# Performance work log

Measured on AMD Instinct MI355X. Metric: run time of the kernel, lower is better.

The kernel has to match this reference:

```python
import jax, jax.numpy as jnp
import numpy as np

I, H, M, C, LOC, K = 512, 256, 80, 1024, 32, 31
C2 = C // 2
B, S, T = 32, 256, 800


def setup_inputs() -> dict:
    key = jax.random.key(0)
    ks = jax.random.split(key, 20)
    sc = 0.02
    return {
        "encodings": jax.random.normal(ks[0], (B, S, I), jnp.float32),
        "queries": jax.random.normal(ks[1], (B, T, H), jnp.float32),
        "outputs": jax.random.normal(ks[2], (B, T, M), jnp.float32),
        "mask": jnp.ones((B, S), jnp.float32),
        # GRUCell (PyTorch layout: gates ordered r, z, n)
        "w_ih": jax.random.normal(ks[3], (3 * C, I + H), jnp.float32) * sc,
        "w_hh": jax.random.normal(ks[4], (3 * C, C), jnp.float32) * sc,
        "b_ih": jax.random.normal(ks[5], (3 * C,), jnp.float32) * sc,
        "b_hh": jax.random.normal(ks[6], (3 * C,), jnp.float32) * sc,
        "w_q": jax.random.normal(ks[7], (C2, C), jnp.float32) * sc,        # proj_query
        "w_loc1": jax.random.normal(ks[8], (LOC, 1, K), jnp.float32) * sc, # Conv1d(1, loc, K)
        "w_loc2": jax.random.normal(ks[9], (C2, LOC), jnp.float32) * sc,   # Conv1d(loc, C2, 1)
        "w_k": jax.random.normal(ks[10], (C2, I), jnp.float32) * sc,       # proj_key
        "b_k": jax.random.normal(ks[11], (C2,), jnp.float32) * sc,
        "w_agg": jax.random.normal(ks[12], (C2,), jnp.float32) * sc,       # Conv1d(C2, 1, 1)
        "w_t1": jax.random.normal(ks[13], (C, I + C + M), jnp.float32) * sc,
        "b_t1": jax.random.normal(ks[14], (C,), jnp.float32) * sc,
        "w_t2": jax.random.normal(ks[15], (C,), jnp.float32) * sc,
    }


def _conv1d(x, w, pad):
    # x: [B, Cin, S], w: [Cout, Cin, K]
    return jax.lax.conv_general_dilated(
        x, w, window_strides=(1,), padding=[(pad, pad)],
        dimension_numbers=("NCH", "OIH", "NCH"))


def _aligner(encodings, queries, outputs, maskb,
             w_ih, w_hh, b_ih, b_hh, w_q, w_loc1, w_loc2, w_k, b_k,
             w_agg, w_t1, b_t1, w_t2):
    bsize, seqlen, _ = encodings.shape
    # key projection: [B, S, C2]
    key = encodings @ w_k.T + b_k
    h0 = jnp.zeros((bsize, C), encodings.dtype)
    align0 = jnp.full((bsize, seqlen), 1.0 / seqlen, encodings.dtype)
    alpha0 = jnp.zeros((bsize, seqlen), encodings.dtype).at[:, 0].set(1.0)
    trans0 = jnp.full((bsize, 1), 0.5, encodings.dtype)

    def step(carry, xt):
        h, align, trans, alpha = carry
        query, frame = xt  # [B,H], [B,M]
        prev = jnp.einsum("bsi,bs->bi", encodings, alpha)
        x = jnp.concatenate([query, prev], axis=-1)  # [B, H+I]
        gx = x @ w_ih.T + b_ih
        gh = h @ w_hh.T + b_hh
        xr, xz, xn = jnp.split(gx, 3, axis=-1)
        hr, hz, hn = jnp.split(gh, 3, axis=-1)
        r = jax.nn.sigmoid(xr + hr)
        z = jax.nn.sigmoid(xz + hz)
        n = jnp.tanh(xn + r * hn)
        h_new = (1.0 - z) * n + z * h  # GRUCell update
        # location features: [B,1,S] -> [B,LOC,S] -> [B,C2,S]
        loc = _conv1d(align[:, None, :], w_loc1, K // 2)
        loc = jnp.einsum("cl,bls->bcs", w_loc2, loc)
        score = loc + (h_new @ w_q.T)[..., None] + key.swapaxes(1, 2)  # [B,C2,S]
        energy = jnp.einsum("c,bcs->bs", w_agg, jnp.tanh(score))
        energy = jnp.where(maskb, -jnp.inf, energy)
        align_new = jax.nn.softmax(energy, axis=-1)
        shifted = jnp.pad(alpha, ((0, 0), (1, 0)))[:, :-1]  # F.pad(alpha, [1,-1])
        alpha_new = ((1.0 - trans) * alpha + trans * shifted + 1e-7) * align_new
        alpha_new = alpha_new / alpha_new.sum(axis=-1, keepdims=True)
        attend = jnp.einsum("bsi,bs->bi", encodings, alpha_new)
        t_in = jnp.concatenate([attend, frame, h_new], axis=-1)
        t = jax.nn.sigmoid(jnp.tanh(t_in @ w_t1.T + b_t1) @ w_t2[:, None])  # [B,1]
        return (h_new, align_new, t, alpha_new), alpha_new

    xs = (queries.swapaxes(0, 1), outputs.swapaxes(0, 1))
    _, alphas = jax.lax.scan(step, (h0, align0, trans0, alpha0), xs)
    return alphas.swapaxes(0, 1)  # [B, T, S]


def reference(encodings, queries, outputs, mask,
              w_ih, w_hh, b_ih, b_hh, w_q, w_loc1, w_loc2, w_k, b_k,
              w_agg, w_t1, b_t1, w_t2):
    maskb = ~(mask.astype(bool))
    return _aligner(encodings, queries, outputs, maskb,
                    w_ih, w_hh, b_ih, b_hh, w_q, w_loc1, w_loc2, w_k, b_k,
                    w_agg, w_t1, b_t1, w_t2)
```

## Files before the change

### kernel.cpp

```cpp
#include <hip/hip_runtime.h>
#include <cstdint>
#include <cstddef>


namespace cfg {
constexpr int NB = 32, NS = 256, NI = 512, NHq = 256, NM = 80;
constexpr int NC = 1024, NC2 = 512, NT = 800;
constexpr int NBLK = 256, NTHR = 512;

constexpr size_t OFF_KEYT  = 0;
constexpr size_t OFF_WKT   = OFF_KEYT + (size_t)NB * NS * NC2;
constexpr size_t OFF_PU    = OFF_WKT + (size_t)NI * NC2;
constexpr size_t OFF_H     = OFF_PU + (size_t)2 * NB * NI;
constexpr size_t OFF_H16   = OFF_H + (size_t)2 * NC * NB;
constexpr size_t OFF_E     = OFF_H16 + (size_t)NB * NC;
constexpr size_t OFF_W     = OFF_E + (size_t)2 * NB * NS;
constexpr size_t OFF_SE    = OFF_W + (size_t)2 * NB * NS;
constexpr size_t OFF_SW    = OFF_SE + 64;
constexpr size_t OFF_TPART = OFF_SW + 64;
constexpr size_t OFF_TRED  = OFF_TPART + (size_t)NBLK * NB;
constexpr size_t OFF_QBUF  = OFF_TRED + 32;
constexpr size_t OFF_BAR   = OFF_QBUF + (size_t)NB * NC2;
constexpr size_t OFF_Q16   = OFF_BAR + 4608;
constexpr size_t OFF_F16   = OFF_Q16 + (size_t)NT * NB * NHq / 2;
constexpr size_t OFF_WQ16  = OFF_F16 + (size_t)NT * NB * 128 / 2;
constexpr size_t WS_FLOATS = OFF_WQ16 + (size_t)NC2 * NC / 2;
}
using namespace cfg;

typedef __attribute__((ext_vector_type(8))) short short8;
typedef __attribute__((ext_vector_type(4))) float f32x4;

#define MF(a, b, c) __builtin_amdgcn_mfma_f32_16x16x32_bf16((a), (b), (c), 0, 0, 0)
#define LDSC(d, p) asm volatile("global_load_dwordx4 %0, %1, off sc0 sc1" : "=v"(d) : "v"(p))

__device__ __forceinline__ float ld_cg(const float* p) {
  return __hip_atomic_load(p, __ATOMIC_RELAXED, __HIP_MEMORY_SCOPE_AGENT);
}
__device__ __forceinline__ void st_cg(float* p, float v) {
  __hip_atomic_store(p, v, __ATOMIC_RELAXED, __HIP_MEMORY_SCOPE_AGENT);
}
// ... 12 lines not shown
               : "+v"(a0), "+v"(a1), "+v"(a2), "+v"(a3), "+v"(a4), "+v"(a5), "+v"(a6), "+v"(a7));
}
__device__ __forceinline__ void vw10(short8& a0, short8& a1, short8& a2, short8& a3, short8& a4,
                                     short8& a5, short8& a6, short8& a7, short8& a8, short8& a9) {
  asm volatile("s_waitcnt vmcnt(0)"
               : "+v"(a0), "+v"(a1), "+v"(a2), "+v"(a3), "+v"(a4), "+v"(a5), "+v"(a6),
                 "+v"(a7), "+v"(a8), "+v"(a9));
}
__device__ __forceinline__ void vw15(short8& a0, short8& a1, short8& a2, short8& a3, short8& a4,
                                     short8& a5, short8& a6, short8& a7, short8& a8, short8& a9,
                                     short8& aa, short8& ab2, short8& ac, short8& ad, short8& ae) {
  asm volatile("s_waitcnt vmcnt(0)"
               : "+v"(a0), "+v"(a1), "+v"(a2), "+v"(a3), "+v"(a4), "+v"(a5), "+v"(a6),
                 "+v"(a7), "+v"(a8), "+v"(a9), "+v"(aa), "+v"(ab2), "+v"(ac), "+v"(ad), "+v"(ae));
}
__device__ __forceinline__ void vw16f(f32x4& a0, f32x4& a1, f32x4& a2, f32x4& a3, f32x4& a4,
                                      f32x4& a5, f32x4& a6, f32x4& a7, f32x4& b0, f32x4& b1,
                                      f32x4& b2, f32x4& b3, f32x4& b4, f32x4& b5, f32x4& b6,
                                      f32x4& b7) {
  asm volatile("s_waitcnt vmcnt(0)"
               : "+v"(a0), "+v"(a1), "+v"(a2), "+v"(a3), "+v"(a4), "+v"(a5), "+v"(a6), "+v"(a7),
                 "+v"(b0), "+v"(b1), "+v"(b2), "+v"(b3), "+v"(b4), "+v"(b5), "+v"(b6), "+v"(b7));
}

__device__ __forceinline__ float frcp(float x) {
#if __has_builtin(__builtin_amdgcn_rcpf)
  return __builtin_amdgcn_rcpf(x);
#else
  return 1.f / x;
#endif
}
__device__ __forceinline__ float fsig(float x) { return frcp(1.f + __expf(-x)); }
__device__ __forceinline__ float ftanh(float x) {
  const float e = __expf(2.f * x);
  return 1.f - 2.f * frcp(e + 1.f);
}
__device__ __forceinline__ short f2bf(float f) {
  unsigned u = __float_as_uint(f);
  u += 0x7FFFu + ((u >> 16) & 1u);
  return (short)(u >> 16);
}
__device__ __forceinline__ float bf2f(short s) {
  return __uint_as_float(((unsigned)(unsigned short)s) << 16);
}
__device__ __forceinline__ short8 cvt8(f32x4 lo, f32x4 hi) {
  short8 a;
  a[0] = f2bf(lo[0]); a[1] = f2bf(lo[1]); a[2] = f2bf(lo[2]); a[3] = f2bf(lo[3]);
  a[4] = f2bf(hi[0]); a[5] = f2bf(hi[1]); a[6] = f2bf(hi[2]); a[7] = f2bf(hi[3]);
  return a;
}

__device__ __forceinline__ void gbarrier(unsigned* root, unsigned* flags, unsigned& ph) {
  ++ph;
  asm volatile("s_waitcnt vmcnt(0)" ::: "memory");
  __syncthreads();
  if (blockIdx.x == 0) {
    const int t = threadIdx.x;
    if (t > 0 && t < 256) {
      while (__hip_atomic_load(&flags[t * 16], __ATOMIC_RELAXED, __HIP_MEMORY_SCOPE_AGENT) < ph)
        __builtin_amdgcn_s_sleep(1);
    }
    __syncthreads();
    if (t == 0)
      __hip_atomic_store(root, ph, __ATOMIC_RELAXED, __HIP_MEMORY_SCOPE_AGENT);
// ... 20 lines not shown
  if (k >= 256 && k < 768) return w_t1[(size_t)c * 1616 + (k - 256)];
  if (k >= 768 && k < 1792) return w_t1[(size_t)c * 1616 + 592 + (k - 768)];
  if (k >= 1792 && k < 1872) return w_t1[(size_t)c * 1616 + 512 + (k - 1792)];
  return 0.f;
}

__global__ void k_init(const float* __restrict__ enc, const float* __restrict__ queries,
                       const float* __restrict__ outputs, const float* __restrict__ w_k,
                       const float* __restrict__ w_q, float* __restrict__ ws) {
  const size_t t0 = (size_t)blockIdx.x * blockDim.x + threadIdx.x;
  const size_t gs = (size_t)gridDim.x * blockDim.x;
  for (size_t x = t0; x < (size_t)NI * NC2; x += gs) {
    const int i = (int)(x / NC2), c2 = (int)(x % NC2);
    ws[OFF_WKT + x] = w_k[(size_t)c2 * NI + i];
  }
  for (size_t x = t0; x < (size_t)NB * NI; x += gs) {
    const int b = (int)(x / NI), i = (int)(x % NI);
    ws[OFF_PU + x] = 0.f;
    ws[OFF_PU + (size_t)NB * NI + b * NI + i] = enc[(size_t)b * NS * NI + i];
  }
  for (size_t x = t0; x < (size_t)2 * NC * NB; x += gs) ws[OFF_H + x] = 0.f;
  for (size_t x = t0; x < (size_t)NB * NC; x += gs) ws[OFF_H16 + x] = 0.f;
  for (size_t x = t0; x < (size_t)NB * NS; x += gs) {
    ws[OFF_E + x] = 0.f;
    ws[OFF_E + (size_t)NB * NS + x] = 1.f;
    ws[OFF_W + x] = 0.f;
    ws[OFF_W + (size_t)NB * NS + x] = ((x & (NS - 1)) == 0) ? 1.f : 0.f;
  }
  for (size_t x = t0; x < (size_t)NB; x += gs) {
    ws[OFF_SE + x] = 0.f; ws[OFF_SE + NB + x] = (float)NS;
    ws[OFF_SW + x] = 0.f; ws[OFF_SW + NB + x] = 1.f;
    ws[OFF_TRED + x] = 0.f;
  }
  unsigned* bar = (unsigned*)(ws + OFF_BAR);
  for (size_t x = t0; x < 4608; x += gs) bar[x] = 0u;
  unsigned short* Q16 = (unsigned short*)(ws + OFF_Q16);
  for (size_t x = t0; x < (size_t)NT * NB * NHq; x += gs) {
    const int k = (int)(x & (NHq - 1));
    const int b = (int)((x >> 8) & (NB - 1));
    const int t = (int)(x >> 13);
    Q16[x] = (unsigned short)f2bf(queries[((size_t)b * NT + t) * NHq + k]);
  }
  unsigned short* F16 = (unsigned short*)(ws + OFF_F16);
  for (size_t x = t0; x < (size_t)NT * NB * 128; x += gs) {
    const int k = (int)(x & 127);
    const int b = (int)((x >> 7) & (NB - 1));
    const int t = (int)(x >> 12);
    F16[x] = (k < NM) ? (unsigned short)f2bf(outputs[((size_t)b * NT + t) * NM + k]) : 0;
  }
  unsigned short* WQ16 = (unsigned short*)(ws + OFF_WQ16);
  for (size_t x = t0; x < (size_t)NC2 * NC; x += gs)
    WQ16[x] = (unsigned short)f2bf(w_q[x]);
}

__global__ __launch_bounds__(NTHR) void k_key(const float* __restrict__ enc,
                                              const float* __restrict__ b_k,
                                              float* __restrict__ ws) {
  __shared__ float encl[4 * NI];
  const int bid = blockIdx.x, tid = threadIdx.x;
  const int b = bid >> 3, s0 = (bid & 7) * 32;
  const float* wkT = ws + OFF_WKT;
  float* keyT = ws + OFF_KEYT;
  const float bk = b_k[tid];
  for (int q = 0; q < 8; ++q) {
    const int sb = s0 + q * 4;
    for (int x = tid; x < 4 * NI; x += NTHR) {
      const int ss = x >> 9, i = x & (NI - 1);
      encl[x] = enc[((size_t)(b * NS + sb + ss)) * NI + i];
    }
    __syncthreads();
    float a0 = bk, a1 = bk, a2 = bk, a3 = bk;
    for (int i = 0; i < NI; ++i) {
      const float wv = wkT[(size_t)i * NC2 + tid];
      a0 += wv * encl[i];           a1 += wv * encl[NI + i];
      a2 += wv * encl[2 * NI + i];  a3 += wv * encl[3 * NI + i];
    }
    keyT[((size_t)(b * NS + sb + 0)) * NC2 + tid] = a0;
    keyT[((size_t)(b * NS + sb + 1)) * NC2 + tid] = a1;
    keyT[((size_t)(b * NS + sb + 2)) * NC2 + tid] = a2;
    keyT[((size_t)(b * NS + sb + 3)) * NC2 + tid] = a3;
    __syncthreads();
  }
}

__global__ __launch_bounds__(NTHR, 2) void k_main(
    const float* __restrict__ enc, const float* __restrict__ mask,
    const float* __restrict__ w_ih, const float* __restrict__ w_hh,
    const float* __restrict__ b_ih, const float* __restrict__ b_hh,
    const float* __restrict__ w_loc1, const float* __restrict__ w_loc2,
    const float* __restrict__ w_agg, const float* __restrict__ w_t1,
    const float* __restrict__ b_t1, const float* __restrict__ w_t2,
    float* ws, float* __restrict__ out) {
  const int bid = blockIdx.x, tid = threadIdx.x;
  float* const keyT = ws + OFF_KEYT;
  float* const PU = ws + OFF_PU;
  float* const HB = ws + OFF_H;
  unsigned short* const HB16 = (unsigned short*)(ws + OFF_H16);
  float* const EB = ws + OFF_E;
  float* const WBUF = ws + OFF_W;
  float* const SEB = ws + OFF_SE;
  float* const SWB = ws + OFF_SW;
  float* const TPART = ws + OFF_TPART;
  float* const TRED = ws + OFF_TRED;
  float* const QBUF = ws + OFF_QBUF;
  unsigned* const root = (unsigned*)(ws + OFF_BAR);
  unsigned* const flags = root + 16;
  const unsigned short* const Q16 = (const unsigned short*)(ws + OFF_Q16);
  const unsigned short* const F16 = (const unsigned short*)(ws + OFF_F16);
  const unsigned short* const WQ16 = (const unsigned short*)(ws + OFF_WQ16);

  __shared__ float Cred[2 * 5 * 4 * 64];
  __shared__ float gout2[5 * 4 * 32];
  __shared__ float swinv_l[32];
  __shared__ float tredl[128];
  __shared__ float alignl[72];
  __shared__ float wl2[34];
  __shared__ float qbl[520];
  __shared__ float Epart[32 * 9];
  __shared__ float wstash[32];
  __shared__ float scal[4];

  const int lane = tid & 63, wv = tid >> 6;
  const int m2 = wv >> 2, k4 = wv & 3;
  const int kg = lane >> 4;
  const int ab = m2 * 16 + (lane & 15);
  const int cs = bid * 4;
  const int pb_b = bid >> 3, pb_s0 = (bid & 7) * 32;
  const int col = lane & 15, quad = lane >> 4;
  unsigned ph = 0;

  short8 wreg[16];
  {
    const int n = lane & 15;
    const int kind = n >> 2, ch = cs + (n & 3);
#pragma unroll
    for (int si = 0; si < 16; ++si) {
      int s = (k4 == 0) ? (si < 8 ? si : (si < 15 ? 16 + si : -1))
            : (k4 == 1) ? 8 + si
            : (k4 == 2) ? (si < 15 ? 31 + si : -1)
                        : (si < 14 ? 46 + si : -1);
      short8 w = {0, 0, 0, 0, 0, 0, 0, 0};
      if (s >= 0) {
        const int k0 = s * 32 + kg * 8;
#pragma unroll
        for (int jj = 0; jj < 8; ++jj)
          w[jj] = f2bf(wcat_val(w_ih, w_hh, w_t1, kind, ch, k0 + jj));
      }
      wreg[si] = w;
    }
  }
  short8 wcA[4];
  unsigned keylo[4][2], keyhi[4][2];
  f32x4 wagr[4];
#pragma unroll
  for (int t = 0; t < 4; ++t) {
    const int mt = 4 * wv + t;
    short8 wfr;
#pragma unroll
    for (int jj = 0; jj < 8; ++jj) {
      const int k = quad * 8 + jj;
      float s = 0.f;
      if (k < 31) {
        const int c2 = mt * 16 + col;
        for (int l = 0; l < 32; ++l) s += w_loc2[c2 * 32 + l] * w_loc1[l * 31 + k];
      }
      wfr[jj] = f2bf(s);
    }
    wcA[t] = wfr;
    const int c2r = mt * 16 + quad * 4;
#pragma unroll
    for (int r = 0; r < 4; ++r) wagr[t][r] = w_agg[c2r + r];
#pragma unroll
    for (int nt = 0; nt < 2; ++nt) {
      const float* kp = &keyT[((size_t)(pb_b * NS + pb_s0 + nt * 16 + col)) * NC2 + c2r];
      keylo[t][nt] = ((unsigned)(unsigned short)f2bf(kp[0])) |
                     (((unsigned)(unsigned short)f2bf(kp[1])) << 16);
      keyhi[t][nt] = ((unsigned)(unsigned short)f2bf(kp[2])) |
                     (((unsigned)(unsigned short)f2bf(kp[3])) << 16);
    }
  }
  if (tid >= 62 && tid < 72) alignl[tid] = 0.f;
  __syncthreads();

  for (int j = 0; j < NT; ++j) {
    const int p = j & 1;
    const float* pu_prev = PU + (size_t)(1 - p) * NB * NI;
    float* pu_cur = PU + (size_t)p * NB * NI;
    const float* h_prev = HB + (size_t)(1 - p) * NC * NB;
    float* h_cur = HB + (size_t)p * NC * NB;
    const unsigned short* hb16_prev = HB16 + (size_t)(1 - p) * NB * NC;
    unsigned short* hb16_cur = HB16 + (size_t)p * NB * NC;
    const float* e_prev = EB + (size_t)(1 - p) * NB * NS;
    float* e_cur = EB + (size_t)p * NB * NS;
    const float* w_prev = WBUF + (size_t)(1 - p) * NB * NS;
    float* w_cur = WBUF + (size_t)p * NB * NS;
    const float* se_prev = SEB + (size_t)(1 - p) * NB;
    float* se_cur = SEB + (size_t)p * NB;
    const float* sw_prev = SWB + (size_t)(1 - p) * NB;
    float* sw_cur = SWB + (size_t)p * NB;

    if (tid < 64) st_cg(&pu_cur[bid * 64 + tid], 0.f);
    if (bid == 0 && tid < NB) st_cg(&se_cur[tid], 0.f);
    if (bid == 1 && tid < NB) st_cg(&sw_cur[tid], 0.f);
    if (tid < NB) swinv_l[tid] = 1.f / ld_cg(&sw_prev[tid]);
    __syncthreads();

    if (j >= 1 && bid < NB && tid < NS)
      out[((size_t)bid * NT + (j - 1)) * NS + tid] = ld_cg(&w_prev[bid * NS + tid]) * swinv_l[bid];

    f32x4 accA = {0.f, 0.f, 0.f, 0.f}, accB = {0.f, 0.f, 0.f, 0.f};
    if (k4 == 0) {
      const unsigned short* qp = Q16 + ((size_t)j * NB + ab) * NHq + kg * 8;
      const unsigned short* hp = hb16_prev + (size_t)ab * NC + kg * 8;
      short8 h0, h1, h2, h3, h4, h5, h6;
      LDSC(h0, hp);        LDSC(h1, hp + 32);   LDSC(h2, hp + 64);  LDSC(h3, hp + 96);
      LDSC(h4, hp + 128);  LDSC(h5, hp + 160);  LDSC(h6, hp + 192);
      const short8 q0 = *(const short8*)(qp);
      const short8 q1 = *(const short8*)(qp + 32);
      const short8 q2 = *(const short8*)(qp + 64);
      const short8 q3 = *(const short8*)(qp + 96);
      const short8 q4 = *(const short8*)(qp + 128);
      const short8 q5 = *(const short8*)(qp + 160);
      const short8 q6 = *(const short8*)(qp + 192);
      const short8 q7 = *(const short8*)(qp + 224);
      vw7(h0, h1, h2, h3, h4, h5, h6);
      accA = MF(q0, wreg[0], accA); accA = MF(q1, wreg[1], accA);
      accA = MF(q2, wreg[2], accA); accA = MF(q3, wreg[3], accA);
      accA = MF(q4, wreg[4], accA); accA = MF(q5, wreg[5], accA);
      accA = MF(q6, wreg[6], accA); accA = MF(q7, wreg[7], accA);
      accB = MF(h0, wreg[8], accB);  accB = MF(h1, wreg[9], accB);
      accB = MF(h2, wreg[10], accB); accB = MF(h3, wreg[11], accB);
      accB = MF(h4, wreg[12], accB); accB = MF(h5, wreg[13], accB);
      accB = MF(h6, wreg[14], accB);
    } else if (k4 == 1) {
      const float* pp = pu_prev + (size_t)ab * NI + kg * 8;
#pragma unroll
      for (int rd = 0; rd < 2; ++rd) {
        const float* pb = pp + rd * 256;
        f32x4 a0, a1, a2, a3, a4, a5, a6, a7, b0, b1, b2, b3, b4, b5, b6, b7;
        LDSC(a0, pb);        LDSC(b0, pb + 4);
        LDSC(a1, pb + 32);   LDSC(b1, pb + 36);
        LDSC(a2, pb + 64);   LDSC(b2, pb + 68);
        LDSC(a3, pb + 96);   LDSC(b3, pb + 100);
        LDSC(a4, pb + 128);  LDSC(b4, pb + 132);
        LDSC(a5, pb + 160);  LDSC(b5, pb + 164);
        LDSC(a6, pb + 192);  LDSC(b6, pb + 196);
        LDSC(a7, pb + 224);  LDSC(b7, pb + 228);
        vw16f(a0, a1, a2, a3, a4, a5, a6, a7, b0, b1, b2, b3, b4, b5, b6, b7);
        const int w0 = rd * 8;
        accA = MF(cvt8(a0, b0), wreg[w0 + 0], accA);
        accA = MF(cvt8(a1, b1), wreg[w0 + 1], accA);
        accA = MF(cvt8(a2, b2), wreg[w0 + 2], accA);
        accA = MF(cvt8(a3, b3), wreg[w0 + 3], accA);
        accA = MF(cvt8(a4, b4), wreg[w0 + 4], accA);
        accA = MF(cvt8(a5, b5), wreg[w0 + 5], accA);
        accA = MF(cvt8(a6, b6), wreg[w0 + 6], accA);
        accA = MF(cvt8(a7, b7), wreg[w0 + 7], accA);
      }
    } else if (k4 == 2) {
      const unsigned short* hp = hb16_prev + (size_t)ab * NC + kg * 8 + 224;
      short8 h0, h1, h2, h3, h4, h5, h6, h7, h8, h9, ha, hb2, hc, hd, he;
      LDSC(h0, hp);        LDSC(h1, hp + 32);  LDSC(h2, hp + 64);  LDSC(h3, hp + 96);
      LDSC(h4, hp + 128);  LDSC(h5, hp + 160); LDSC(h6, hp + 192); LDSC(h7, hp + 224);
      LDSC(h8, hp + 256);  LDSC(h9, hp + 288); LDSC(ha, hp + 320); LDSC(hb2, hp + 352);
      LDSC(hc, hp + 384);  LDSC(hd, hp + 416); LDSC(he, hp + 448);
      vw15(h0, h1, h2, h3, h4, h5, h6, h7, h8, h9, ha, hb2, hc, hd, he);
      accA = MF(h0, wreg[0], accA);  accA = MF(h1, wreg[1], accA);
      accA = MF(h2, wreg[2], accA);  accA = MF(h3, wreg[3], accA);
      accA = MF(h4, wreg[4], accA);  accA = MF(h5, wreg[5], accA);
      accA = MF(h6, wreg[6], accA);  accA = MF(h7, wreg[7], accA);
      accA = MF(h8, wreg[8], accA);  accA = MF(h9, wreg[9], accA);
      accA = MF(ha, wreg[10], accA); accA = MF(hb2, wreg[11], accA);
      accA = MF(hc, wreg[12], accA); accA = MF(hd, wreg[13], accA);
// ... 32 lines not shown
      } else {
        const int sg = 1 + k4;
#pragma unroll
        for (int r = 0; r < 4; ++r) Cred[cidx(m2, sg, r, lane)] = accA[r];
      }
    }
    __syncthreads();
    {
      const int n = tid & 15, b = tid >> 4;
      const int m2r = b >> 4, bm = b & 15, l = (bm >> 2) * 16 + n, r = bm & 3;
      auto cidx = [](int m, int sg, int rr, int ll) { return ((m * 5 + sg) * 4 + rr) * 64 + ll; };
      const float s0 = Cred[cidx(m2r, 0, r, l)];
      const float sB = Cred[cidx(m2r, 1, r, l)];
      const float s1 = Cred[cidx(m2r, 2, r, l)];
      const float s2 = sB + Cred[cidx(m2r, 3, r, l)] + Cred[cidx(m2r, 4, r, l)];
      const float swv = swinv_l[b];
      const int kind = n >> 2, c4o = n & 3;
      if (kind == 2) {
        gout2[2 * 128 + c4o * 32 + b] = s0 + swv * s1;
        gout2[3 * 128 + c4o * 32 + b] = s2;
      } else {
        const int slot = (kind == 3) ? 4 : kind;
        gout2[slot * 128 + c4o * 32 + b] = s0 + swv * s1 + s2;
      }
    }
    __syncthreads();
    if (tid < 128) {
      const int c4o = tid >> 5, b = tid & 31, c = cs + c4o;
      const float xr = gout2[0 * 128 + c4o * 32 + b] + b_ih[c] + b_hh[c];
      const float xz = gout2[1 * 128 + c4o * 32 + b] + b_ih[NC + c] + b_hh[NC + c];
      const float xn = gout2[2 * 128 + c4o * 32 + b] + b_ih[2 * NC + c];
      const float hn = gout2[3 * 128 + c4o * 32 + b] + b_hh[2 * NC + c];
      const float tp = gout2[4 * 128 + c4o * 32 + b];
      const float r = fsig(xr), z = fsig(xz);
      const float nn = ftanh(xn + r * hn);
      const float hnew = (1.f - z) * nn + z * h_prev[c * 32 + b];
      h_cur[c * 32 + b] = hnew;
      st_cg_u16(&hb16_cur[(size_t)b * NC + c], (unsigned short)f2bf(hnew));
      tredl[c4o * 32 + b] = w_t2[c] * ftanh(tp + b_t1[c]);
    }
    __syncthreads();
    if (tid < NB)
      st_cg(&TPART[bid * NB + tid],
            tredl[tid] + tredl[32 + tid] + tredl[64 + tid] + tredl[96 + tid]);
    gbarrier(root, flags, ph);

    if (bid < 32) {
      f32x4 qacc = {0.f, 0.f, 0.f, 0.f};
      const unsigned short* hb = HB16 + (size_t)p * NB * NC + (size_t)ab * NC + kg * 8;
      short8 g0, g1, g2, g3, g4, g5, g6, g7;
      LDSC(g0, hb + (k4 * 8 + 0) * 32); LDSC(g1, hb + (k4 * 8 + 1) * 32);
      LDSC(g2, hb + (k4 * 8 + 2) * 32); LDSC(g3, hb + (k4 * 8 + 3) * 32);
      LDSC(g4, hb + (k4 * 8 + 4) * 32); LDSC(g5, hb + (k4 * 8 + 5) * 32);
      LDSC(g6, hb + (k4 * 8 + 6) * 32); LDSC(g7, hb + (k4 * 8 + 7) * 32);
      const int jq = bid * 16 + col;
      const unsigned short* wp = WQ16 + (size_t)jq * NC + k4 * 8 * 32 + kg * 8;
      vw8(g0, g1, g2, g3, g4, g5, g6, g7);
      qacc = MF(g0, *(const short8*)(wp), qacc);
      qacc = MF(g1, *(const short8*)(wp + 32), qacc);
      qacc = MF(g2, *(const short8*)(wp + 64), qacc);
      qacc = MF(g3, *(const short8*)(wp + 96), qacc);
      qacc = MF(g4, *(const short8*)(wp + 128), qacc);
      qacc = MF(g5, *(const short8*)(wp + 160), qacc);
      qacc = MF(g6, *(const short8*)(wp + 192), qacc);
      qacc = MF(g7, *(const short8*)(wp + 224), qacc);
#pragma unroll
      for (int r = 0; r < 4; ++r) Cred[((m2 * 4 + k4) * 4 + r) * 64 + lane] = qacc[r];
      __syncthreads();
      {
        const int col2 = tid & 15, b2 = tid >> 4;
        const int m2r = b2 >> 4, bm = b2 & 15, l = (bm >> 2) * 16 + col2, r = bm & 3;
        float s = 0.f;
#pragma unroll
        for (int kk = 0; kk < 4; ++kk) s += Cred[((m2r * 4 + kk) * 4 + r) * 64 + l];
        st_cg(&QBUF[(size_t)b2 * NC2 + bid * 16 + col2], s);
      }
    } else if (bid >= 64 && bid < 96) {
      const int b2 = bid - 64;
      float v = (tid < NBLK) ? ld_cg(&TPART[tid * NB + b2]) : 0.f;
#pragma unroll
      for (int off = 32; off > 0; off >>= 1) v += __shfl_down(v, off);
      if (lane == 0) Cred[wv] = v;
      __syncthreads();
      if (tid == 0) {
        float s = 0.f;
#pragma unroll
        for (int w8 = 0; w8 < 8; ++w8) s += Cred[w8];
        st_cg(&TRED[b2], s);
      }
    }
    gbarrier(root, flags, ph);

    {
      const int b = pb_b, s0v = pb_s0;
      if (tid == 0) {
        scal[0] = ld_cg(&se_prev[b]);
        scal[1] = ld_cg(&sw_prev[b]);
        scal[2] = ld_cg(&TRED[b]);
      }
      qbl[tid] = ld_cg(&QBUF[(size_t)b * NC2 + tid]);
      if (tid < 62) {
        const int sp = s0v + tid - 15;
        alignl[tid] = (sp >= 0 && sp < NS) ? ld_cg(&e_prev[b * NS + sp]) : 0.f;
      }
      if (tid >= 64 && tid < 97) {
        const int i2 = tid - 64, sp = s0v + i2 - 1;
        wl2[i2] = (sp >= 0 && sp < NS) ? ld_cg(&w_prev[b * NS + sp]) : 0.f;
      }
      __syncthreads();
      const float invSE = 1.f / scal[0];
      const float invSW = 1.f / scal[1];
      const float tr = (j == 0) ? 0.5f : fsig(scal[2]);
      short8 bfr[2];
#pragma unroll
      for (int nt = 0; nt < 2; ++nt) {
        const int base = nt * 16 + col + quad * 8;
        short8 bv;
#pragma unroll
        for (int jj = 0; jj < 8; ++jj) bv[jj] = f2bf(alignl[base + jj] * invSE);
        bfr[nt] = bv;
      }
#pragma unroll
      for (int nt = 0; nt < 2; ++nt) {
        float pe = 0.f;
#pragma unroll
        for (int t = 0; t < 4; ++t) {
          const int c2b = (4 * wv + t) * 16 + quad * 4;
          f32x4 acc;
          acc[0] = qbl[c2b + 0] + __uint_as_float(keylo[t][nt] << 16);
          acc[1] = qbl[c2b + 1] + __uint_as_float(keylo[t][nt] & 0xffff0000u);
          acc[2] = qbl[c2b + 2] + __uint_as_float(keyhi[t][nt] << 16);
          acc[3] = qbl[c2b + 3] + __uint_as_float(keyhi[t][nt] & 0xffff0000u);
          acc = MF(wcA[t], bfr[nt], acc);
          pe += wagr[t][0] * ftanh(acc[0]);
          pe += wagr[t][1] * ftanh(acc[1]);
          pe += wagr[t][2] * ftanh(acc[2]);
          pe += wagr[t][3] * ftanh(acc[3]);
        }
        pe += __shfl_xor(pe, 16);
        pe += __shfl_xor(pe, 32);
        if (lane < 16) Epart[(nt * 16 + col) * 9 + wv] = pe;
      }
      __syncthreads();
      if (tid < 32) {
        const int sl = tid, s = s0v + sl;
        float Ev = 0.f;
#pragma unroll
        for (int w8 = 0; w8 < 8; ++w8) Ev += Epart[sl * 9 + w8];
        const float ev = (mask[b * NS + s] != 0.f) ? __expf(Ev) : 0.f;
        const float csv = ((1.f - tr) * wl2[sl + 1] + tr * wl2[sl]) * invSW + 1e-7f;
        const float wvv = csv * ev;
        st_cg(&e_cur[b * NS + s], ev);
        st_cg(&w_cur[b * NS + s], wvv);
        wstash[sl] = wvv;
        float se = ev, sw2 = wvv;
#pragma unroll
        for (int off = 16; off > 0; off >>= 1) {
          se += __shfl_down(se, off, 32);
          sw2 += __shfl_down(sw2, off, 32);
        }
        if (sl == 0) { atomicAdd(&se_cur[b], se); atomicAdd(&sw_cur[b], sw2); }
      }
      __syncthreads();
      {
        float acc = 0.f;
        const float* encb = enc + ((size_t)(b * NS + s0v)) * NI + tid;
#pragma unroll 8
        for (int ss = 0; ss < 32; ++ss) acc += wstash[ss] * encb[(size_t)ss * NI];
        atomicAdd(&pu_cur[(size_t)b * NI + tid], acc);
      }
    }
    gbarrier(root, flags, ph);
  }

  if (bid < NB && tid < NS) {
    const float invSW = 1.f / ld_cg(&SWB[NB + bid]);
    out[((size_t)bid * NT + (NT - 1)) * NS + tid] =
        ld_cg(&WBUF[(size_t)NB * NS + bid * NS + tid]) * invSW;
  }
}

extern "C" void kernel_launch(void* const* d_in, const int* in_sizes, int n_in,
                              void* d_out, int out_size, void* d_ws, size_t ws_size,
                              hipStream_t stream) {
  const float* enc     = (const float*)d_in[0];
  const float* queries = (const float*)d_in[1];
  const float* outputs = (const float*)d_in[2];
  const float* mask    = (const float*)d_in[3];
  const float* w_ih    = (const float*)d_in[4];
  const float* w_hh    = (const float*)d_in[5];
  const float* b_ih    = (const float*)d_in[6];
  const float* b_hh    = (const float*)d_in[7];
  const float* w_q     = (const float*)d_in[8];
// ... 19 lines not shown
```

Measured before the change: 21.28 ms.

## Restructure attention phase to one block per batch, dropping a grid barrier per step

The attention phase moves from 256 blocks (8 per batch row) to 32 blocks that each own a whole batch row. The query projection, transition reduction, softmax and alpha normalization are computed locally, which removes one grid-wide barrier per timestep plus the cross-block atomics and global buffers for the e/w sums. Encodings, keys and the attended vector are stored in bf16 to halve memory traffic. The cost is that 224 blocks sit idle during this phase, each active block does eight times more work serially, and there is extra bf16 rounding of attend and encodings.

```diff
diff --git a/kernel.cpp b/kernel.cpp
--- a/kernel.cpp
+++ b/kernel.cpp
@@ -8,23 +8,18 @@
 constexpr int NC = 1024, NC2 = 512, NT = 800;
 constexpr int NBLK = 256, NTHR = 512;
 
-constexpr size_t OFF_KEYT  = 0;
-constexpr size_t OFF_WKT   = OFF_KEYT + (size_t)NB * NS * NC2;
-constexpr size_t OFF_PU    = OFF_WKT + (size_t)NI * NC2;
-constexpr size_t OFF_H     = OFF_PU + (size_t)2 * NB * NI;
+constexpr size_t OFF_WKT   = 0;
+constexpr size_t OFF_PU16  = OFF_WKT + (size_t)NI * NC2;
+constexpr size_t OFF_H     = OFF_PU16 + (size_t)NB * NC2;
 constexpr size_t OFF_H16   = OFF_H + (size_t)2 * NC * NB;
-constexpr size_t OFF_E     = OFF_H16 + (size_t)NB * NC;
-constexpr size_t OFF_W     = OFF_E + (size_t)2 * NB * NS;
-constexpr size_t OFF_SE    = OFF_W + (size_t)2 * NB * NS;
-constexpr size_t OFF_SW    = OFF_SE + 64;
-constexpr size_t OFF_TPART = OFF_SW + 64;
-constexpr size_t OFF_TRED  = OFF_TPART + (size_t)NBLK * NB;
-constexpr size_t OFF_QBUF  = OFF_TRED + 32;
-constexpr size_t OFF_BAR   = OFF_QBUF + (size_t)NB * NC2;
+constexpr size_t OFF_TPART = OFF_H16 + (size_t)NB * NC;
+constexpr size_t OFF_BAR   = OFF_TPART + (size_t)NBLK * NB;
 constexpr size_t OFF_Q16   = OFF_BAR + 4608;
 constexpr size_t OFF_F16   = OFF_Q16 + (size_t)NT * NB * NHq / 2;
 constexpr size_t OFF_WQ16  = OFF_F16 + (size_t)NT * NB * 128 / 2;
-constexpr size_t WS_FLOATS = OFF_WQ16 + (size_t)NC2 * NC / 2;
+constexpr size_t OFF_KEY16 = OFF_WQ16 + (size_t)NC2 * NC / 2;
+constexpr size_t OFF_ENC16 = OFF_KEY16 + (size_t)NB * NS * NC2 / 2;
+constexpr size_t WS_FLOATS = OFF_ENC16 + (size_t)NB * NS * NI / 2;
 }
 using namespace cfg;
 
@@ -67,14 +62,6 @@
                : "+v"(a0), "+v"(a1), "+v"(a2), "+v"(a3), "+v"(a4), "+v"(a5), "+v"(a6),
                  "+v"(a7), "+v"(a8), "+v"(a9), "+v"(aa), "+v"(ab2), "+v"(ac), "+v"(ad), "+v"(ae));
 }
-__device__ __forceinline__ void vw16f(f32x4& a0, f32x4& a1, f32x4& a2, f32x4& a3, f32x4& a4,
-                                      f32x4& a5, f32x4& a6, f32x4& a7, f32x4& b0, f32x4& b1,
-                                      f32x4& b2, f32x4& b3, f32x4& b4, f32x4& b5, f32x4& b6,
-                                      f32x4& b7) {
-  asm volatile("s_waitcnt vmcnt(0)"
-               : "+v"(a0), "+v"(a1), "+v"(a2), "+v"(a3), "+v"(a4), "+v"(a5), "+v"(a6), "+v"(a7),
-                 "+v"(b0), "+v"(b1), "+v"(b2), "+v"(b3), "+v"(b4), "+v"(b5), "+v"(b6), "+v"(b7));
-}
 
 __device__ __forceinline__ float frcp(float x) {
 #if __has_builtin(__builtin_amdgcn_rcpf)
@@ -93,14 +80,8 @@
   u += 0x7FFFu + ((u >> 16) & 1u);
   return (short)(u >> 16);
 }
-__device__ __forceinline__ float bf2f(short s) {
-  return __uint_as_float(((unsigned)(unsigned short)s) << 16);
-}
-__device__ __forceinline__ short8 cvt8(f32x4 lo, f32x4 hi) {
-  short8 a;
-  a[0] = f2bf(lo[0]); a[1] = f2bf(lo[1]); a[2] = f2bf(lo[2]); a[3] = f2bf(lo[3]);
-  a[4] = f2bf(hi[0]); a[5] = f2bf(hi[1]); a[6] = f2bf(hi[2]); a[7] = f2bf(hi[3]);
-  return a;
+__device__ __forceinline__ float bfu(unsigned short u) {
+  return __uint_as_float(((unsigned)u) << 16);
 }
 
 __device__ __forceinline__ void gbarrier(unsigned* root, unsigned* flags, unsigned& ph) {
@@ -151,24 +132,15 @@
     const int i = (int)(x / NC2), c2 = (int)(x % NC2);
     ws[OFF_WKT + x] = w_k[(size_t)c2 * NI + i];
   }
-  for (size_t x = t0; x < (size_t)NB * NI; x += gs) {
-    const int b = (int)(x / NI), i = (int)(x % NI);
-    ws[OFF_PU + x] = 0.f;
-    ws[OFF_PU + (size_t)NB * NI + b * NI + i] = enc[(size_t)b * NS * NI + i];
+  unsigned short* PU16 = (unsigned short*)(ws + OFF_PU16);
+  for (size_t x = t0; x < (size_t)NB * NC2; x += gs) {
+    const int b = (int)(x / NC2), i = (int)(x % NC2);
+    PU16[x] = 0;
+    PU16[(size_t)NB * NC2 + x] = (unsigned short)f2bf(enc[(size_t)b * NS * NI + i]);
   }
   for (size_t x = t0; x < (size_t)2 * NC * NB; x += gs) ws[OFF_H + x] = 0.f;
   for (size_t x = t0; x < (size_t)NB * NC; x += gs) ws[OFF_H16 + x] = 0.f;
-  for (size_t x = t0; x < (size_t)NB * NS; x += gs) {
-    ws[OFF_E + x] = 0.f;
-    ws[OFF_E + (size_t)NB * NS + x] = 1.f;
-    ws[OFF_W + x] = 0.f;
-    ws[OFF_W + (size_t)NB * NS + x] = ((x & (NS - 1)) == 0) ? 1.f : 0.f;
-  }
-  for (size_t x = t0; x < (size_t)NB; x += gs) {
-    ws[OFF_SE + x] = 0.f; ws[OFF_SE + NB + x] = (float)NS;
-    ws[OFF_SW + x] = 0.f; ws[OFF_SW + NB + x] = 1.f;
-    ws[OFF_TRED + x] = 0.f;
-  }
+  for (size_t x = t0; x < (size_t)NBLK * NB; x += gs) ws[OFF_TPART + x] = 0.f;
   unsigned* bar = (unsigned*)(ws + OFF_BAR);
   for (size_t x = t0; x < 4608; x += gs) bar[x] = 0u;
   unsigned short* Q16 = (unsigned short*)(ws + OFF_Q16);
@@ -188,6 +160,9 @@
   unsigned short* WQ16 = (unsigned short*)(ws + OFF_WQ16);
   for (size_t x = t0; x < (size_t)NC2 * NC; x += gs)
     WQ16[x] = (unsigned short)f2bf(w_q[x]);
+  unsigned short* ENC16 = (unsigned short*)(ws + OFF_ENC16);
+  for (size_t x = t0; x < (size_t)NB * NS * NI; x += gs)
+    ENC16[x] = (unsigned short)f2bf(enc[x]);
 }
 
 __global__ __launch_bounds__(NTHR) void k_key(const float* __restrict__ enc,
@@ -197,7 +172,7 @@
   const int bid = blockIdx.x, tid = threadIdx.x;
   const int b = bid >> 3, s0 = (bid & 7) * 32;
   const float* wkT = ws + OFF_WKT;
-  float* keyT = ws + OFF_KEYT;
+  unsigned short* KEY16 = (unsigned short*)(ws + OFF_KEY16);
   const float bk = b_k[tid];
   for (int q = 0; q < 8; ++q) {
     const int sb = s0 + q * 4;
@@ -212,10 +187,10 @@
       a0 += wv * encl[i];           a1 += wv * encl[NI + i];
       a2 += wv * encl[2 * NI + i];  a3 += wv * encl[3 * NI + i];
     }
-    keyT[((size_t)(b * NS + sb + 0)) * NC2 + tid] = a0;
-    keyT[((size_t)(b * NS + sb + 1)) * NC2 + tid] = a1;
-    keyT[((size_t)(b * NS + sb + 2)) * NC2 + tid] = a2;
-    keyT[((size_t)(b * NS + sb + 3)) * NC2 + tid] = a3;
+    KEY16[((size_t)(b * NS + sb + 0)) * NC2 + tid] = (unsigned short)f2bf(a0);
+    KEY16[((size_t)(b * NS + sb + 1)) * NC2 + tid] = (unsigned short)f2bf(a1);
+    KEY16[((size_t)(b * NS + sb + 2)) * NC2 + tid] = (unsigned short)f2bf(a2);
+    KEY16[((size_t)(b * NS + sb + 3)) * NC2 + tid] = (unsigned short)f2bf(a3);
     __syncthreads();
   }
 }
@@ -229,40 +204,35 @@
     const float* __restrict__ b_t1, const float* __restrict__ w_t2,
     float* ws, float* __restrict__ out) {
   const int bid = blockIdx.x, tid = threadIdx.x;
-  float* const keyT = ws + OFF_KEYT;
-  float* const PU = ws + OFF_PU;
   float* const HB = ws + OFF_H;
   unsigned short* const HB16 = (unsigned short*)(ws + OFF_H16);
-  float* const EB = ws + OFF_E;
-  float* const WBUF = ws + OFF_W;
-  float* const SEB = ws + OFF_SE;
-  float* const SWB = ws + OFF_SW;
+  unsigned short* const PU16 = (unsigned short*)(ws + OFF_PU16);
   float* const TPART = ws + OFF_TPART;
-  float* const TRED = ws + OFF_TRED;
-  float* const QBUF = ws + OFF_QBUF;
   unsigned* const root = (unsigned*)(ws + OFF_BAR);
   unsigned* const flags = root + 16;
   const unsigned short* const Q16 = (const unsigned short*)(ws + OFF_Q16);
   const unsigned short* const F16 = (const unsigned short*)(ws + OFF_F16);
   const unsigned short* const WQ16 = (const unsigned short*)(ws + OFF_WQ16);
+  const unsigned short* const KEY16 = (const unsigned short*)(ws + OFF_KEY16);
+  const unsigned short* const ENC16 = (const unsigned short*)(ws + OFF_ENC16);
 
   __shared__ float Cred[2 * 5 * 4 * 64];
   __shared__ float gout2[5 * 4 * 32];
-  __shared__ float swinv_l[32];
   __shared__ float tredl[128];
-  __shared__ float alignl[72];
-  __shared__ float wl2[34];
-  __shared__ float qbl[520];
-  __shared__ float Epart[32 * 9];
-  __shared__ float wstash[32];
-  __shared__ float scal[4];
+  __shared__ float redA[256], redB[256];
+  __shared__ float qL[512];
+  __shared__ float eLp[288];
+  __shared__ float wLp[260];
+  __shared__ float alphaL[256];
+  __shared__ float Epart[256 * 8];
+  __shared__ float scal[8];
+  __shared__ __align__(16) unsigned short hL[1024];
 
   const int lane = tid & 63, wv = tid >> 6;
   const int m2 = wv >> 2, k4 = wv & 3;
   const int kg = lane >> 4;
   const int ab = m2 * 16 + (lane & 15);
   const int cs = bid * 4;
-  const int pb_b = bid >> 3, pb_s0 = (bid & 7) * 32;
   const int col = lane & 15, quad = lane >> 4;
   unsigned ph = 0;
 
@@ -287,7 +257,6 @@
     }
   }
   short8 wcA[4];
-  unsigned keylo[4][2], keyhi[4][2];
   f32x4 wagr[4];
 #pragma unroll
   for (int t = 0; t < 4; ++t) {
@@ -307,43 +276,22 @@
     const int c2r = mt * 16 + quad * 4;
 #pragma unroll
     for (int r = 0; r < 4; ++r) wagr[t][r] = w_agg[c2r + r];
-#pragma unroll
-    for (int nt = 0; nt < 2; ++nt) {
-      const float* kp = &keyT[((size_t)(pb_b * NS + pb_s0 + nt * 16 + col)) * NC2 + c2r];
-      keylo[t][nt] = ((unsigned)(unsigned short)f2bf(kp[0])) |
-                     (((unsigned)(unsigned short)f2bf(kp[1])) << 16);
-      keyhi[t][nt] = ((unsigned)(unsigned short)f2bf(kp[2])) |
-                     (((unsigned)(unsigned short)f2bf(kp[3])) << 16);
-    }
-  }
-  if (tid >= 62 && tid < 72) alignl[tid] = 0.f;
+  }
+  if (bid < NB) {
+    if (tid < 288) eLp[tid] = (tid >= 15 && tid < 271) ? 1.f : 0.f;
+    if (tid < 260) wLp[tid] = (tid == 1) ? 1.f : 0.f;
+    if (tid == 0) { scal[0] = (float)NS; scal[1] = 1.f; }
+  }
   __syncthreads();
 
   for (int j = 0; j < NT; ++j) {
     const int p = j & 1;
-    const float* pu_prev = PU + (size_t)(1 - p) * NB * NI;
-    float* pu_cur = PU + (size_t)p * NB * NI;
     const float* h_prev = HB + (size_t)(1 - p) * NC * NB;
     float* h_cur = HB + (size_t)p * NC * NB;
     const unsigned short* hb16_prev = HB16 + (size_t)(1 - p) * NB * NC;
     unsigned short* hb16_cur = HB16 + (size_t)p * NB * NC;
-    const float* e_prev = EB + (size_t)(1 - p) * NB * NS;
-    float* e_cur = EB + (size_t)p * NB * NS;
-    const float* w_prev = WBUF + (size_t)(1 - p) * NB * NS;
-    float* w_cur = WBUF + (size_t)p * NB * NS;
-    const float* se_prev = SEB + (size_t)(1 - p) * NB;
-    float* se_cur = SEB + (size_t)p * NB;
-    const float* sw_prev = SWB + (size_t)(1 - p) * NB;
-    float* sw_cur = SWB + (size_t)p * NB;
-
-    if (tid < 64) st_cg(&pu_cur[bid * 64 + tid], 0.f);
-    if (bid == 0 && tid < NB) st_cg(&se_cur[tid], 0.f);
-    if (bid == 1 && tid < NB) st_cg(&sw_cur[tid], 0.f);
-    if (tid < NB) swinv_l[tid] = 1.f / ld_cg(&sw_prev[tid]);
-    __syncthreads();
-
-    if (j >= 1 && bid < NB && tid < NS)
-      out[((size_t)bid * NT + (j - 1)) * NS + tid] = ld_cg(&w_prev[bid * NS + tid]) * swinv_l[bid];
+    const unsigned short* pu16_prev = PU16 + (size_t)(1 - p) * NB * NC2;
+    unsigned short* pu16_cur = PU16 + (size_t)p * NB * NC2;
 
     f32x4 accA = {0.f, 0.f, 0.f, 0.f}, accB = {0.f, 0.f, 0.f, 0.f};
     if (k4 == 0) {
@@ -370,30 +318,23 @@
       accB = MF(h4, wreg[12], accB); accB = MF(h5, wreg[13], accB);
       accB = MF(h6, wreg[14], accB);
     } else if (k4 == 1) {
-      const float* pp = pu_prev + (size_t)ab * NI + kg * 8;
-#pragma unroll
-      for (int rd = 0; rd < 2; ++rd) {
-        const float* pb = pp + rd * 256;
-        f32x4 a0, a1, a2, a3, a4, a5, a6, a7, b0, b1, b2, b3, b4, b5, b6, b7;
-        LDSC(a0, pb);        LDSC(b0, pb + 4);
-        LDSC(a1, pb + 32);   LDSC(b1, pb + 36);
-        LDSC(a2, pb + 64);   LDSC(b2, pb + 68);
-        LDSC(a3, pb + 96);   LDSC(b3, pb + 100);
-        LDSC(a4, pb + 128);  LDSC(b4, pb + 132);
-        LDSC(a5, pb + 160);  LDSC(b5, pb + 164);
-        LDSC(a6, pb + 192);  LDSC(b6, pb + 196);
-        LDSC(a7, pb + 224);  LDSC(b7, pb + 228);
-        vw16f(a0, a1, a2, a3, a4, a5, a6, a7, b0, b1, b2, b3, b4, b5, b6, b7);
-        const int w0 = rd * 8;
-        accA = MF(cvt8(a0, b0), wreg[w0 + 0], accA);
-        accA = MF(cvt8(a1, b1), wreg[w0 + 1], accA);
-        accA = MF(cvt8(a2, b2), wreg[w0 + 2], accA);
-        accA = MF(cvt8(a3, b3), wreg[w0 + 3], accA);
-        accA = MF(cvt8(a4, b4), wreg[w0 + 4], accA);
-        accA = MF(cvt8(a5, b5), wreg[w0 + 5], accA);
-        accA = MF(cvt8(a6, b6), wreg[w0 + 6], accA);
-        accA = MF(cvt8(a7, b7), wreg[w0 + 7], accA);
-      }
+      const unsigned short* pp = pu16_prev + (size_t)ab * NC2 + kg * 8;
+      short8 u0, u1, u2, u3, u4, u5, u6, u7;
+      LDSC(u0, pp);        LDSC(u1, pp + 32);  LDSC(u2, pp + 64);  LDSC(u3, pp + 96);
+      LDSC(u4, pp + 128);  LDSC(u5, pp + 160); LDSC(u6, pp + 192); LDSC(u7, pp + 224);
+      vw8(u0, u1, u2, u3, u4, u5, u6, u7);
+      accA = MF(u0, wreg[0], accA); accA = MF(u1, wreg[1], accA);
+      accA = MF(u2, wreg[2], accA); accA = MF(u3, wreg[3], accA);
+      accA = MF(u4, wreg[4], accA); accA = MF(u5, wreg[5], accA);
+      accA = MF(u6, wreg[6], accA); accA = MF(u7, wreg[7], accA);
+      short8 v0, v1, v2, v3, v4, v5, v6, v7;
+      LDSC(v0, pp + 256);  LDSC(v1, pp + 288); LDSC(v2, pp + 320); LDSC(v3, pp + 352);
+      LDSC(v4, pp + 384);  LDSC(v5, pp + 416); LDSC(v6, pp + 448); LDSC(v7, pp + 480);
+      vw8(v0, v1, v2, v3, v4, v5, v6, v7);
+      accA = MF(v0, wreg[8], accA);  accA = MF(v1, wreg[9], accA);
+      accA = MF(v2, wreg[10], accA); accA = MF(v3, wreg[11], accA);
+      accA = MF(v4, wreg[12], accA); accA = MF(v5, wreg[13], accA);
+      accA = MF(v6, wreg[14], accA); accA = MF(v7, wreg[15], accA);
     } else if (k4 == 2) {
       const unsigned short* hp = hb16_prev + (size_t)ab * NC + kg * 8 + 224;
       short8 h0, h1, h2, h3, h4, h5, h6, h7, h8, h9, ha, hb2, hc, hd, he;
@@ -456,14 +397,13 @@
       const float sB = Cred[cidx(m2r, 1, r, l)];
       const float s1 = Cred[cidx(m2r, 2, r, l)];
       const float s2 = sB + Cred[cidx(m2r, 3, r, l)] + Cred[cidx(m2r, 4, r, l)];
-      const float swv = swinv_l[b];
       const int kind = n >> 2, c4o = n & 3;
       if (kind == 2) {
-        gout2[2 * 128 + c4o * 32 + b] = s0 + swv * s1;
+        gout2[2 * 128 + c4o * 32 + b] = s0 + s1;
         gout2[3 * 128 + c4o * 32 + b] = s2;
       } else {
         const int slot = (kind == 3) ? 4 : kind;
-        gout2[slot * 128 + c4o * 32 + b] = s0 + swv * s1 + s2;
+        gout2[slot * 128 + c4o * 32 + b] = s0 + s1 + s2;
       }
     }
     __syncthreads();
@@ -487,138 +427,129 @@
             tredl[tid] + tredl[32 + tid] + tredl[64 + tid] + tredl[96 + tid]);
     gbarrier(root, flags, ph);
 
-    if (bid < 32) {
-      f32x4 qacc = {0.f, 0.f, 0.f, 0.f};
-      const unsigned short* hb = HB16 + (size_t)p * NB * NC + (size_t)ab * NC + kg * 8;
-      short8 g0, g1, g2, g3, g4, g5, g6, g7;
-      LDSC(g0, hb + (k4 * 8 + 0) * 32); LDSC(g1, hb + (k4 * 8 + 1) * 32);
-      LDSC(g2, hb + (k4 * 8 + 2) * 32); LDSC(g3, hb + (k4 * 8 + 3) * 32);
-      LDSC(g4, hb + (k4 * 8 + 4) * 32); LDSC(g5, hb + (k4 * 8 + 5) * 32);
-      LDSC(g6, hb + (k4 * 8 + 6) * 32); LDSC(g7, hb + (k4 * 8 + 7) * 32);
-      const int jq = bid * 16 + col;
-      const unsigned short* wp = WQ16 + (size_t)jq * NC + k4 * 8 * 32 + kg * 8;
-      vw8(g0, g1, g2, g3, g4, g5, g6, g7);
-      qacc = MF(g0, *(const short8*)(wp), qacc);
-      qacc = MF(g1, *(const short8*)(wp + 32), qacc);
-      qacc = MF(g2, *(const short8*)(wp + 64), qacc);
-      qacc = MF(g3, *(const short8*)(wp + 96), qacc);
-      qacc = MF(g4, *(const short8*)(wp + 128), qacc);
-      qacc = MF(g5, *(const short8*)(wp + 160), qacc);
-      qacc = MF(g6, *(const short8*)(wp + 192), qacc);
-      qacc = MF(g7, *(const short8*)(wp + 224), qacc);
-#pragma unroll
-      for (int r = 0; r < 4; ++r) Cred[((m2 * 4 + k4) * 4 + r) * 64 + lane] = qacc[r];
+    if (bid < NB) {
+      const int b = bid;
+      if (tid < 128) {
+        short8 hv;
+        LDSC(hv, hb16_cur + (size_t)b * NC + tid * 8);
+        asm volatile("s_waitcnt vmcnt(0)" : "+v"(hv));
+        *(short8*)&hL[tid * 8] = hv;
+      }
+      if (tid < 256) redA[tid] = ld_cg(&TPART[tid * NB + b]);
+      __syncthreads();
+      if (tid < 64) {
+        float s = redA[tid] + redA[tid + 64] + redA[tid + 128] + redA[tid + 192];
+#pragma unroll
+        for (int off = 32; off > 0; off >>= 1) s += __shfl_xor(s, off);
+        if (tid == 0) scal[2] = s;
+      }
+      {
+        const unsigned short* wp0 = WQ16 + (size_t)((4 * wv + 0) * 16 + col) * NC + kg * 8;
+        const unsigned short* wp1 = WQ16 + (size_t)((4 * wv + 1) * 16 + col) * NC + kg * 8;
+        const unsigned short* wp2 = WQ16 + (size_t)((4 * wv + 2) * 16 + col) * NC + kg * 8;
+        const unsigned short* wp3 = WQ16 + (size_t)((4 * wv + 3) * 16 + col) * NC + kg * 8;
+        f32x4 qa0 = {0.f,0.f,0.f,0.f}, qa1 = qa0, qa2 = qa0, qa3 = qa0;
+#pragma unroll 4
+        for (int kk = 0; kk < 32; ++kk) {
+          short8 aF = {0, 0, 0, 0, 0, 0, 0, 0};
+          if ((lane & 15) == 0) aF = *(const short8*)&hL[kk * 32 + kg * 8];
+          qa0 = MF(aF, *(const short8*)(wp0 + kk * 32), qa0);
+          qa1 = MF(aF, *(const short8*)(wp1 + kk * 32), qa1);
+          qa2 = MF(aF, *(const short8*)(wp2 + kk * 32), qa2);
+          qa3 = MF(aF, *(const short8*)(wp3 + kk * 32), qa3);
+        }
+        if (lane < 16) {
+          qL[(4 * wv + 0) * 16 + lane] = qa0[0];
+          qL[(4 * wv + 1) * 16 + lane] = qa1[0];
+          qL[(4 * wv + 2) * 16 + lane] = qa2[0];
+          qL[(4 * wv + 3) * 16 + lane] = qa3[0];
+        }
+      }
       __syncthreads();
       {
-        const int col2 = tid & 15, b2 = tid >> 4;
-        const int m2r = b2 >> 4, bm = b2 & 15, l = (bm >> 2) * 16 + col2, r = bm & 3;
-        float s = 0.f;
-#pragma unroll
-        for (int kk = 0; kk < 4; ++kk) s += Cred[((m2r * 4 + kk) * 4 + r) * 64 + l];
-        st_cg(&QBUF[(size_t)b2 * NC2 + bid * 16 + col2], s);
-      }
-    } else if (bid >= 64 && bid < 96) {
-      const int b2 = bid - 64;
-      float v = (tid < NBLK) ? ld_cg(&TPART[tid * NB + b2]) : 0.f;
-#pragma unroll
-      for (int off = 32; off > 0; off >>= 1) v += __shfl_down(v, off);
-      if (lane == 0) Cred[wv] = v;
-      __syncthreads();
-      if (tid == 0) {
-        float s = 0.f;
-#pragma unroll
-        for (int w8 = 0; w8 < 8; ++w8) s += Cred[w8];
-        st_cg(&TRED[b2], s);
-      }
-    }
-    gbarrier(root, flags, ph);
-
-    {
-      const int b = pb_b, s0v = pb_s0;
-      if (tid == 0) {
-        scal[0] = ld_cg(&se_prev[b]);
-        scal[1] = ld_cg(&sw_prev[b]);
-        scal[2] = ld_cg(&TRED[b]);
-      }
-      qbl[tid] = ld_cg(&QBUF[(size_t)b * NC2 + tid]);
-      if (tid < 62) {
-        const int sp = s0v + tid - 15;
-        alignl[tid] = (sp >= 0 && sp < NS) ? ld_cg(&e_prev[b * NS + sp]) : 0.f;
-      }
-      if (tid >= 64 && tid < 97) {
-        const int i2 = tid - 64, sp = s0v + i2 - 1;
-        wl2[i2] = (sp >= 0 && sp < NS) ? ld_cg(&w_prev[b * NS + sp]) : 0.f;
-      }
-      __syncthreads();
-      const float invSE = 1.f / scal[0];
-      const float invSW = 1.f / scal[1];
-      const float tr = (j == 0) ? 0.5f : fsig(scal[2]);
-      short8 bfr[2];
-#pragma unroll
-      for (int nt = 0; nt < 2; ++nt) {
-        const int base = nt * 16 + col + quad * 8;
-        short8 bv;
-#pragma unroll
-        for (int jj = 0; jj < 8; ++jj) bv[jj] = f2bf(alignl[base + jj] * invSE);
-        bfr[nt] = bv;
-      }
-#pragma unroll
-      for (int nt = 0; nt < 2; ++nt) {
-        float pe = 0.f;
+        const float invSE = 1.f / scal[0];
+        float qv[4][4];
 #pragma unroll
         for (int t = 0; t < 4; ++t) {
           const int c2b = (4 * wv + t) * 16 + quad * 4;
-          f32x4 acc;
-          acc[0] = qbl[c2b + 0] + __uint_as_float(keylo[t][nt] << 16);
-          acc[1] = qbl[c2b + 1] + __uint_as_float(keylo[t][nt] & 0xffff0000u);
-          acc[2] = qbl[c2b + 2] + __uint_as_float(keyhi[t][nt] << 16);
-          acc[3] = qbl[c2b + 3] + __uint_as_float(keyhi[t][nt] & 0xffff0000u);
-          acc = MF(wcA[t], bfr[nt], acc);
-          pe += wagr[t][0] * ftanh(acc[0]);
-          pe += wagr[t][1] * ftanh(acc[1]);
-          pe += wagr[t][2] * ftanh(acc[2]);
-          pe += wagr[t][3] * ftanh(acc[3]);
-        }
-        pe += __shfl_xor(pe, 16);
-        pe += __shfl_xor(pe, 32);
-        if (lane < 16) Epart[(nt * 16 + col) * 9 + wv] = pe;
+#pragma unroll
+          for (int r = 0; r < 4; ++r) qv[t][r] = qL[c2b + r];
+        }
+        for (int ns = 0; ns < 16; ++ns) {
+          const int sbase = ns * 16 + col + kg * 8;
+          short8 bF;
+#pragma unroll
+          for (int jj = 0; jj < 8; ++jj) bF[jj] = f2bf(eLp[sbase + jj] * invSE);
+          float pe = 0.f;
+#pragma unroll
+          for (int t = 0; t < 4; ++t) {
+            const uint2 kv = *(const uint2*)(KEY16 +
+                ((size_t)(b * NS + ns * 16 + col)) * NC2 + (4 * wv + t) * 16 + quad * 4);
+            f32x4 acc;
+            acc[0] = __uint_as_float(kv.x << 16)          + qv[t][0];
+            acc[1] = __uint_as_float(kv.x & 0xffff0000u)  + qv[t][1];
+            acc[2] = __uint_as_float(kv.y << 16)          + qv[t][2];
+            acc[3] = __uint_as_float(kv.y & 0xffff0000u)  + qv[t][3];
+            acc = MF(wcA[t], bF, acc);
+            pe += wagr[t][0] * ftanh(acc[0]);
+            pe += wagr[t][1] * ftanh(acc[1]);
+            pe += wagr[t][2] * ftanh(acc[2]);
+            pe += wagr[t][3] * ftanh(acc[3]);
+          }
+          pe += __shfl_xor(pe, 16);
+          pe += __shfl_xor(pe, 32);
+          if (lane < 16) Epart[(ns * 16 + col) * 8 + wv] = pe;
+        }
       }
       __syncthreads();
-      if (tid < 32) {
-        const int sl = tid, s = s0v + sl;
+      const float tr = (j == 0) ? 0.5f : fsig(scal[2]);
+      const float invSWold = 1.f / scal[1];
+      if (tid < 256) {
         float Ev = 0.f;
 #pragma unroll
-        for (int w8 = 0; w8 < 8; ++w8) Ev += Epart[sl * 9 + w8];
-        const float ev = (mask[b * NS + s] != 0.f) ? __expf(Ev) : 0.f;
-        const float csv = ((1.f - tr) * wl2[sl + 1] + tr * wl2[sl]) * invSW + 1e-7f;
-        const float wvv = csv * ev;
-        st_cg(&e_cur[b * NS + s], ev);
-        st_cg(&w_cur[b * NS + s], wvv);
-        wstash[sl] = wvv;
-        float se = ev, sw2 = wvv;
-#pragma unroll
-        for (int off = 16; off > 0; off >>= 1) {
-          se += __shfl_down(se, off, 32);
-          sw2 += __shfl_down(sw2, off, 32);
-        }
-        if (sl == 0) { atomicAdd(&se_cur[b], se); atomicAdd(&sw_cur[b], sw2); }
+        for (int w8 = 0; w8 < 8; ++w8) Ev += Epart[tid * 8 + w8];
+        const float ev = (mask[b * NS + tid] != 0.f) ? __expf(Ev) : 0.f;
+        const float csv = ((1.f - tr) * wLp[1 + tid] + tr * wLp[tid]) * invSWold + 1e-7f;
+        redA[tid] = ev;
+        redB[tid] = csv * ev;
+      }
+      __syncthreads();
+      if (tid < 64) {
+        float sa = redA[tid] + redA[tid + 64] + redA[tid + 128] + redA[tid + 192];
+        float sb = redB[tid] + redB[tid + 64] + redB[tid + 128] + redB[tid + 192];
+#pragma unroll
+        for (int off = 32; off > 0; off >>= 1) {
+          sa += __shfl_xor(sa, off);
+          sb += __shfl_xor(sb, off);
+        }
+        if (tid == 0) { scal[3] = sa; scal[4] = sb; }
+      }
+      __syncthreads();
+      const float invSWnew = 1.f / scal[4];
+      if (tid < 256) {
+        eLp[15 + tid] = redA[tid];
+        wLp[1 + tid] = redB[tid];
+        const float al = redB[tid] * invSWnew;
+        alphaL[tid] = al;
+        out[((size_t)b * NT + j) * NS + tid] = al;
       }
       __syncthreads();
       {
-        float acc = 0.f;
-        const float* encb = enc + ((size_t)(b * NS + s0v)) * NI + tid;
-#pragma unroll 8
-        for (int ss = 0; ss < 32; ++ss) acc += wstash[ss] * encb[(size_t)ss * NI];
-        atomicAdd(&pu_cur[(size_t)b * NI + tid], acc);
-      }
+        const unsigned short* ep = ENC16 + (size_t)b * NS * NI + tid;
+        float a0 = 0.f, a1 = 0.f, a2 = 0.f, a3 = 0.f;
+#pragma unroll 2
+        for (int s = 0; s < 256; s += 4) {
+          a0 += alphaL[s + 0] * bfu(ep[(size_t)(s + 0) * NI]);
+          a1 += alphaL[s + 1] * bfu(ep[(size_t)(s + 1) * NI]);
+          a2 += alphaL[s + 2] * bfu(ep[(size_t)(s + 2) * NI]);
+          a3 += alphaL[s + 3] * bfu(ep[(size_t)(s + 3) * NI]);
+        }
+        const float pu = (a0 + a1) + (a2 + a3);
+        st_cg_u16(&pu16_cur[(size_t)b * NC2 + tid], (unsigned short)f2bf(pu));
+      }
+      if (tid == 0) { scal[0] = scal[3]; scal[1] = scal[4]; }
     }
     gbarrier(root, flags, ph);
-  }
-
-  if (bid < NB && tid < NS) {
-    const float invSW = 1.f / ld_cg(&SWB[NB + bid]);
-    out[((size_t)bid * NT + (NT - 1)) * NS + tid] =
-        ld_cg(&WBUF[(size_t)NB * NS + bid * NS + tid]) * invSW;
   }
 }
 
```

After: 47.63 ms. +123.8%, slower.
